# Kernel tuning notes

Hardware: AMD Instinct MI355X
Metric: run time of the kernel (lower is better)

Reference implementation:

```python
import jax, jax.numpy as jnp
import numpy as np

B, C, H, L, D = 128, 5, 50, 32, 300
VOCAB = 50000
KN = 20  # len(torch.arange(-0.9, 1.1, 0.1))
EPS = 1e-8


def setup_inputs() -> dict:
    key = jax.random.key(0)
    k1, k2, k3, k4 = jax.random.split(key, 4)
    return {
        "candidate_title": jax.random.randint(k1, (B, C, L), 0, VOCAB),
        "clicked_title": jax.random.randint(k2, (B, H, L), 0, VOCAB),
        "embedding": jax.random.normal(k3, (VOCAB, D), dtype=jnp.float32),
        "ltr_w": jax.random.normal(k4, (1, H * KN), dtype=jnp.float32) * 0.03,
        "ltr_b": jnp.zeros((1,), dtype=jnp.float32),
    }


def reference(candidate_title, clicked_title, embedding, ltr_w, ltr_b):
    mus = jnp.arange(KN, dtype=jnp.float32) * 0.1 - 0.9
    sigmas = jnp.concatenate([jnp.full((KN - 1,), 0.1, dtype=jnp.float32),
                              jnp.array([0.001], dtype=jnp.float32)])

    ce = embedding[candidate_title]            # [B,C,L,D]
    he = embedding[clicked_title]              # [B,H,L,D]
    # torch CosineSimilarity: dot / (clamp(||a||,eps)*clamp(||b||,eps))
    cn = ce / jnp.clip(jnp.linalg.norm(ce, axis=-1, keepdims=True), EPS)
    hn = he / jnp.clip(jnp.linalg.norm(he, axis=-1, keepdims=True), EPS)
    sim = jnp.einsum('bcid,bhjd->bchij', cn, hn)  # [B,C,H,L,L] fusion matrix

    # kernel pooling: sum over columns j per Gaussian kernel, then log-sum over rows i
    pooled = jnp.stack(
        [jnp.sum(jnp.exp(-(sim - mus[k]) ** 2 / (2.0 * sigmas[k] ** 2)), axis=-1)
         for k in range(KN)], axis=-1)          # [B,C,H,L,KN]
    pv = jnp.sum(jnp.log(jnp.clip(pooled, 1e-10)), axis=-2)  # [B,C,H,KN]
    pv = pv.reshape(B, C, H * KN)

    score = pv @ ltr_w.T + ltr_b               # [B,C,1]
    return jax.nn.log_softmax(score, axis=1)[..., 0]  # [B,C]
```

## Files before the change

kernel.cpp:

```cpp
#include <hip/hip_runtime.h>
#include <hip/hip_bf16.h>

#define VOCABN 50000
#define BN 128
#define CN 5
#define HN 50
#define LN 32
#define DN 300
#define DP 320
#define KNN 20

typedef __bf16    bf16x8 __attribute__((ext_vector_type(8)));
typedef float     f32x4  __attribute__((ext_vector_type(4)));
typedef float     f32x2  __attribute__((ext_vector_type(2)));
typedef ushort    u16x8  __attribute__((ext_vector_type(8)));

#if __has_builtin(__builtin_amdgcn_exp2f)
#define FEXP2 __builtin_amdgcn_exp2f
#else
#define FEXP2 exp2f
#endif
#if __has_builtin(__builtin_amdgcn_logf)
#define FLOG2 __builtin_amdgcn_logf
#else
#define FLOG2 log2f
#endif

#define LOG2E 1.4426950408889634f
#define LN2F  0.6931471805599453f

__global__ __launch_bounds__(256) void knorm_embed2(const float* __restrict__ emb,
                                                    ushort* __restrict__ tabo) {
    const int t    = threadIdx.x;
    const int lane = t & 63;
    const int w    = t >> 6;
    const int v    = blockIdx.x * 4 + w;
    const float* row = emb + (size_t)v * DN;
    const float4* r4 = (const float4*)row;

    float4 x = r4[lane];
    float ss = x.x * x.x + x.y * x.y + x.z * x.z + x.w * x.w;
    if (lane < 11) {
        float4 y = r4[64 + lane];
        ss += y.x * y.x + y.y * y.y + y.z * y.z + y.w * y.w;
    }
    #pragma unroll
    for (int off = 32; off; off >>= 1) ss += __shfl_xor(ss, off);
    const float scale = 1.0f / fmaxf(sqrtf(ss), 1e-8f);

    if (lane < 40) {
        u16x8 u;
        #pragma unroll
        for (int j = 0; j < 8; ++j) {
            int e = lane * 8 + j;
            float f = (e < DN) ? row[e] * scale : 0.f;
            __hip_bfloat16 h = __float2bfloat16(f);
            u[j] = *(ushort*)&h;
        }
        *(u16x8*)(tabo + (size_t)v * DP + lane * 8) = u;
    }
}

__device__ __forceinline__ int paddr(int row, int c) {
    return ((row >> 1) << 7) + ((((c + ((row & 1) << 2))) ^ ((row >> 1) & 7)) << 4);
}
__device__ __forceinline__ bf16x8 ldP(const ushort* buf, int row, int c) {
    return *(const bf16x8*)((const char*)buf + paddr(row, c));
}

__global__ __launch_bounds__(320, 4) void knrm_fused7(const int* __restrict__ cand,
                                                      const int* __restrict__ clik,
                                                      const ushort* __restrict__ tab,
                                                      const float* __restrict__ ltr_w,
                                                      float* __restrict__ score) {
    __shared__ __align__(16) ushort Abuf[2][80 * 64];
    __shared__ __align__(16) ushort Bbuf[2][32 * 64];
    __shared__ int tokA[160];
    __shared__ int tokB[64];

    const int t    = threadIdx.x;
    const int lane = t & 63;
    const int w    = t >> 6;
    const int bid  = (blockIdx.x & 7) * 400 + (blockIdx.x >> 3);
    const int b    = bid / 25;
    const int hg   = bid % 25;
    const int h0   = hg * 2;

    if (t < 160)      tokA[t] = cand[b * (CN * LN) + t];
    else if (t < 224) tokB[t - 160] = clik[b * (HN * LN) + h0 * LN + (t - 160)];
    __syncthreads();

    const int m15 = lane & 15;
    const int g4  = lane >> 4;

    const char* srcA[2]; int dstA[2];
    #pragma unroll
    for (int it = 0; it < 2; ++it) {
        int cid = it * 320 + t, ar = cid >> 2, c = cid & 3;
        srcA[it] = (const char*)tab + (size_t)tokA[ar] * (DP * 2) + c * 16;
        dstA[it] = paddr(ar, c);
    }
    const char* srcB; int dstB;
    {
        int tb = (t < 256) ? t : (t - 64);
        int ar = tb >> 2, c = tb & 3;
        srcB = (const char*)tab + (size_t)tokB[ar] * (DP * 2) + c * 16;
        dstB = paddr(ar, c);
    }

    f32x4 acc[2][4];
    #pragma unroll
    for (int at = 0; at < 2; ++at)
        #pragma unroll
        for (int jg = 0; jg < 4; ++jg)
            acc[at][jg] = (f32x4){0.f, 0.f, 0.f, 0.f};

    {
        int4 a0 = *(const int4*)(srcA[0]);
        int4 a1 = *(const int4*)(srcA[1]);
        int4 b0; if (t < 256) b0 = *(const int4*)(srcB);
        *(int4*)((char*)&Abuf[0][0] + dstA[0]) = a0;
        *(int4*)((char*)&Abuf[0][0] + dstA[1]) = a1;
        if (t < 256) *(int4*)((char*)&Bbuf[0][0] + dstB) = b0;
    }
    __syncthreads();

    #pragma unroll 2
    for (int ss = 0; ss < 10; ++ss) {
        const ushort* A = &Abuf[ss & 1][0];
        const ushort* B = &Bbuf[ss & 1][0];

        int4 a0, a1, b0;
        if (ss < 9) {
            const int so = (ss + 1) * 64;
            a0 = *(const int4*)(srcA[0] + so);
            a1 = *(const int4*)(srcA[1] + so);
            if (t < 256) b0 = *(const int4*)(srcB + so);
        }

        bf16x8 af0 = ldP(A, w * 32 + m15,      g4);
        bf16x8 af1 = ldP(A, w * 32 + 16 + m15, g4);
        #pragma unroll
        for (int jg = 0; jg < 4; ++jg) {
            bf16x8 bf = ldP(B, jg * 16 + m15, g4);
            acc[0][jg] = __builtin_amdgcn_mfma_f32_16x16x32_bf16(af0, bf, acc[0][jg], 0, 0, 0);
            acc[1][jg] = __builtin_amdgcn_mfma_f32_16x16x32_bf16(af1, bf, acc[1][jg], 0, 0, 0);
        }

        if (ss < 9) {
            char* An = (char*)&Abuf[(ss + 1) & 1][0];
            char* Bn = (char*)&Bbuf[(ss + 1) & 1][0];
            *(int4*)(An + dstA[0]) = a0;
            *(int4*)(An + dstA[1]) = a1;
            if (t < 256) *(int4*)(Bn + dstB) = b0;
            __syncthreads();
        }
    }

    const float C1   = 10.0f * LOG2E;
    const float C2   = -50.0f * LOG2E;
    const float AK19 = 849.3218002880191f;
    static const float CkT[10] = {
        1.0f, 0.6065306597126334f, 0.1353352832366127f, 0.011108996538242306f,
        3.3546262790251185e-4f, 3.7266531720786709e-6f, 1.5229979744712628e-8f,
        2.2897348456191135e-11f, 1.2664165549094176e-14f, 2.576757109154981e-18f };

    float* sb = (w < 4) ? ((float*)&Abuf[0][0] + w * (16 * 33))
                        : ((float*)&Bbuf[0][0]);
    const float* sp0 = sb + (lane >> 2) * 33 + (lane & 3) * 8;
    float res = 0.f;

    #pragma unroll
    for (int hl = 0; hl < 2; ++hl) {
        const float* wrow = ltr_w + (h0 + hl) * KNN;
        #pragma unroll
        for (int at = 0; at < 2; ++at) {
            #pragma unroll
            for (int r = 0; r < 4; ++r) {
                sb[(g4 * 4 + r) * 33 + m15]      = acc[at][hl * 2][r];
                sb[(g4 * 4 + r) * 33 + 16 + m15] = acc[at][hl * 2 + 1][r];
            }

            f32x2 Qp[9];
            #pragma unroll
            for (int j = 0; j < 9; ++j) Qp[j] = (f32x2){0.f, 0.f};
            float Q9 = 0.f, Q19 = 0.f;

            #pragma unroll
            for (int e = 0; e < 8; ++e) {
                float s  = sp0[e];
                float cs = C1 * s;
                float tt = FEXP2(cs);
                float uu = FEXP2(-cs);
                float e0 = FEXP2(C2 * (s * s));
                Q9 += e0;
                f32x2 tu = {tt, uu};
                f32x2 pm = {e0, e0};
                #pragma unroll
                for (int j = 0; j < 9; ++j) { pm *= tu; Qp[j] += pm; }
                float d = fmaf(s, AK19, -AK19);
                Q19 += FEXP2(-(d * d));
            }
            #pragma unroll
            for (int j = 0; j < 9; ++j) {
                Qp[j].x += __shfl_xor(Qp[j].x, 1); Qp[j].x += __shfl_xor(Qp[j].x, 2);
                Qp[j].y += __shfl_xor(Qp[j].y, 1); Qp[j].y += __shfl_xor(Qp[j].y, 2);
            }
            Q9  += __shfl_xor(Q9, 1);  Q9  += __shfl_xor(Q9, 2);
            Q19 += __shfl_xor(Q19, 1); Q19 += __shfl_xor(Q19, 2);

            float rs = wrow[9] * FLOG2(fmaxf(Q9, 1e-10f));
            #pragma unroll
            for (int j = 1; j <= 9; ++j) {
                rs += wrow[9 + j] * FLOG2(fmaxf(Qp[j - 1].x * CkT[j], 1e-10f));
                rs += wrow[9 - j] * FLOG2(fmaxf(Qp[j - 1].y * CkT[j], 1e-10f));
            }
            rs += wrow[19] * FLOG2(fmaxf(Q19, 1e-10f));
            res += rs;
        }
    }

    res *= 0.25f * LN2F;
    #pragma unroll
    for (int off = 32; off; off >>= 1) res += __shfl_xor(res, off);
    if (lane == 0) atomicAdd(&score[b * CN + w], res);
}

__global__ __launch_bounds__(128) void knrm_final(const float* __restrict__ score,
                                                  float* __restrict__ out) {
    int b = threadIdx.x;
    if (b < BN) {
        float s[CN];
        float m = -1e30f;
        #pragma unroll
        for (int c = 0; c < CN; ++c) { s[c] = score[b * CN + c]; m = fmaxf(m, s[c]); }
        float sum = 0.f;
        #pragma unroll
        for (int c = 0; c < CN; ++c) sum += FEXP2((s[c] - m) * LOG2E);
        float lse = m + FLOG2(sum) * LN2F;
        #pragma unroll
        for (int c = 0; c < CN; ++c) out[b * CN + c] = s[c] - lse;
    }
}

extern "C" void kernel_launch(void* const* d_in, const int* in_sizes, int n_in,
                              void* d_out, int out_size, void* d_ws, size_t ws_size,
                              hipStream_t stream) {
    const int*   cand  = (const int*)d_in[0];
    const int*   clik  = (const int*)d_in[1];
    const float* emb   = (const float*)d_in[2];
    const float* ltr_w = (const float*)d_in[3];
    float* out = (float*)d_out;

    const size_t TAB_B = (size_t)VOCABN * DP * 2;

    ushort* tab  = (ushort*)d_ws;
    float*  scre = (float*)((char*)d_ws + TAB_B);

    hipMemsetAsync(scre, 0, BN * CN * sizeof(float), stream);
    knorm_embed2<<<VOCABN / 4, 256, 0, stream>>>(emb, tab);
    knrm_fused7<<<BN * 25, 320, 0, stream>>>(cand, clik, tab, ltr_w, scre);
    knrm_final<<<1, 128, 0, stream>>>(scre, out);
}
```

Measured before the change: 129.6 us.

## Process one clicked title per block and split pooling rows across half-waves

Each block now handles a single clicked history title instead of two. That doubles the grid to BN*HN blocks, halves the B tile, per-thread accumulators and shared memory, and raises the launch-bounds occupancy hint from 4 to 6. The kernel-pooling epilogue is restructured so each of the 64 lanes reduces one full row over 16 columns with vectorized LDS reads, using one cross-half shuffle instead of 4-lane shuffle trees. In exchange, the candidate A tile is reloaded from global memory twice as often per clicked title, since the candidate tokens are re-gathered per block.

```diff
diff --git a/kernel.cpp b/kernel.cpp
--- a/kernel.cpp
+++ b/kernel.cpp
@@ -68,26 +68,28 @@
     return *(const bf16x8*)((const char*)buf + paddr(row, c));
 }
 
-__global__ __launch_bounds__(320, 4) void knrm_fused7(const int* __restrict__ cand,
+__global__ __launch_bounds__(320, 6) void knrm_fused8(const int* __restrict__ cand,
                                                       const int* __restrict__ clik,
                                                       const ushort* __restrict__ tab,
                                                       const float* __restrict__ ltr_w,
                                                       float* __restrict__ score) {
-    __shared__ __align__(16) ushort Abuf[2][80 * 64];
-    __shared__ __align__(16) ushort Bbuf[2][32 * 64];
-    __shared__ int tokA[160];
-    __shared__ int tokB[64];
+    __shared__ __align__(16) char smem[25344];
+    ushort* Abuf0 = (ushort*)smem;
+    ushort* Abuf1 = (ushort*)(smem + 10240);
+    ushort* Bbuf0 = (ushort*)(smem + 20480);
+    ushort* Bbuf1 = (ushort*)(smem + 22528);
+    int*    tokA  = (int*)(smem + 24576);
+    int*    tokB  = (int*)(smem + 25216);
 
     const int t    = threadIdx.x;
     const int lane = t & 63;
     const int w    = t >> 6;
-    const int bid  = (blockIdx.x & 7) * 400 + (blockIdx.x >> 3);
-    const int b    = bid / 25;
-    const int hg   = bid % 25;
-    const int h0   = hg * 2;
+    const int bid  = (blockIdx.x & 7) * 800 + (blockIdx.x >> 3);
+    const int b    = bid / HN;
+    const int h    = bid % HN;
 
     if (t < 160)      tokA[t] = cand[b * (CN * LN) + t];
-    else if (t < 224) tokB[t - 160] = clik[b * (HN * LN) + h0 * LN + (t - 160)];
+    else if (t < 192) tokB[t - 160] = clik[b * (HN * LN) + h * LN + (t - 160)];
     __syncthreads();
 
     const int m15 = lane & 15;
@@ -102,60 +104,61 @@
     }
     const char* srcB; int dstB;
     {
-        int tb = (t < 256) ? t : (t - 64);
+        int tb = t & 127;
         int ar = tb >> 2, c = tb & 3;
         srcB = (const char*)tab + (size_t)tokB[ar] * (DP * 2) + c * 16;
         dstB = paddr(ar, c);
     }
 
-    f32x4 acc[2][4];
+    f32x4 acc[2][2];
     #pragma unroll
     for (int at = 0; at < 2; ++at)
         #pragma unroll
-        for (int jg = 0; jg < 4; ++jg)
+        for (int jg = 0; jg < 2; ++jg)
             acc[at][jg] = (f32x4){0.f, 0.f, 0.f, 0.f};
 
     {
         int4 a0 = *(const int4*)(srcA[0]);
         int4 a1 = *(const int4*)(srcA[1]);
-        int4 b0; if (t < 256) b0 = *(const int4*)(srcB);
-        *(int4*)((char*)&Abuf[0][0] + dstA[0]) = a0;
-        *(int4*)((char*)&Abuf[0][0] + dstA[1]) = a1;
-        if (t < 256) *(int4*)((char*)&Bbuf[0][0] + dstB) = b0;
+        int4 b0; if (t < 128) b0 = *(const int4*)(srcB);
+        *(int4*)((char*)Abuf0 + dstA[0]) = a0;
+        *(int4*)((char*)Abuf0 + dstA[1]) = a1;
+        if (t < 128) *(int4*)((char*)Bbuf0 + dstB) = b0;
     }
     __syncthreads();
 
     #pragma unroll 2
     for (int ss = 0; ss < 10; ++ss) {
-        const ushort* A = &Abuf[ss & 1][0];
-        const ushort* B = &Bbuf[ss & 1][0];
+        const ushort* A = (ss & 1) ? Abuf1 : Abuf0;
+        const ushort* B = (ss & 1) ? Bbuf1 : Bbuf0;
 
         int4 a0, a1, b0;
         if (ss < 9) {
             const int so = (ss + 1) * 64;
             a0 = *(const int4*)(srcA[0] + so);
             a1 = *(const int4*)(srcA[1] + so);
-            if (t < 256) b0 = *(const int4*)(srcB + so);
+            if (t < 128) b0 = *(const int4*)(srcB + so);
         }
 
         bf16x8 af0 = ldP(A, w * 32 + m15,      g4);
         bf16x8 af1 = ldP(A, w * 32 + 16 + m15, g4);
-        #pragma unroll
-        for (int jg = 0; jg < 4; ++jg) {
-            bf16x8 bf = ldP(B, jg * 16 + m15, g4);
-            acc[0][jg] = __builtin_amdgcn_mfma_f32_16x16x32_bf16(af0, bf, acc[0][jg], 0, 0, 0);
-            acc[1][jg] = __builtin_amdgcn_mfma_f32_16x16x32_bf16(af1, bf, acc[1][jg], 0, 0, 0);
-        }
+        bf16x8 bf0 = ldP(B, m15,      g4);
+        bf16x8 bf1 = ldP(B, 16 + m15, g4);
+        acc[0][0] = __builtin_amdgcn_mfma_f32_16x16x32_bf16(af0, bf0, acc[0][0], 0, 0, 0);
+        acc[0][1] = __builtin_amdgcn_mfma_f32_16x16x32_bf16(af0, bf1, acc[0][1], 0, 0, 0);
+        acc[1][0] = __builtin_amdgcn_mfma_f32_16x16x32_bf16(af1, bf0, acc[1][0], 0, 0, 0);
+        acc[1][1] = __builtin_amdgcn_mfma_f32_16x16x32_bf16(af1, bf1, acc[1][1], 0, 0, 0);
 
         if (ss < 9) {
-            char* An = (char*)&Abuf[(ss + 1) & 1][0];
-            char* Bn = (char*)&Bbuf[(ss + 1) & 1][0];
+            char* An = (char*)((ss & 1) ? Abuf0 : Abuf1);
+            char* Bn = (char*)((ss & 1) ? Bbuf0 : Bbuf1);
             *(int4*)(An + dstA[0]) = a0;
             *(int4*)(An + dstA[1]) = a1;
-            if (t < 256) *(int4*)(Bn + dstB) = b0;
+            if (t < 128) *(int4*)(Bn + dstB) = b0;
             __syncthreads();
         }
     }
+    __syncthreads();
 
     const float C1   = 10.0f * LOG2E;
     const float C2   = -50.0f * LOG2E;
@@ -165,62 +168,64 @@
         3.3546262790251185e-4f, 3.7266531720786709e-6f, 1.5229979744712628e-8f,
         2.2897348456191135e-11f, 1.2664165549094176e-14f, 2.576757109154981e-18f };
 
-    float* sb = (w < 4) ? ((float*)&Abuf[0][0] + w * (16 * 33))
-                        : ((float*)&Bbuf[0][0]);
-    const float* sp0 = sb + (lane >> 2) * 33 + (lane & 3) * 8;
-    float res = 0.f;
-
-    #pragma unroll
-    for (int hl = 0; hl < 2; ++hl) {
-        const float* wrow = ltr_w + (h0 + hl) * KNN;
-        #pragma unroll
-        for (int at = 0; at < 2; ++at) {
+    float* sb = (float*)(smem + w * 4224);
+
+    #pragma unroll
+    for (int at = 0; at < 2; ++at)
+        #pragma unroll
+        for (int jgl = 0; jgl < 2; ++jgl)
             #pragma unroll
-            for (int r = 0; r < 4; ++r) {
-                sb[(g4 * 4 + r) * 33 + m15]      = acc[at][hl * 2][r];
-                sb[(g4 * 4 + r) * 33 + 16 + m15] = acc[at][hl * 2 + 1][r];
-            }
-
-            f32x2 Qp[9];
+            for (int r = 0; r < 4; ++r)
+                sb[(at * 16 + g4 * 4 + r) * 33 + jgl * 16 + m15] = acc[at][jgl][r];
+
+    const int hi = lane >> 5;
+    const float* sp = sb + (lane & 31) * 33 + hi * 16;
+
+    f32x2 Qp[9];
+    #pragma unroll
+    for (int j = 0; j < 9; ++j) Qp[j] = (f32x2){0.f, 0.f};
+    float Q9 = 0.f, Q19 = 0.f;
+
+    #pragma unroll
+    for (int ec = 0; ec < 4; ++ec) {
+        f32x4 v = *(const f32x4*)(sp + ec * 4);
+        #pragma unroll
+        for (int e = 0; e < 4; ++e) {
+            float s  = v[e];
+            float cs = C1 * s;
+            float tt = FEXP2(cs);
+            float uu = FEXP2(-cs);
+            float e0 = FEXP2(C2 * (s * s));
+            Q9 += e0;
+            f32x2 tu = {tt, uu};
+            f32x2 pm = {e0, e0};
             #pragma unroll
-            for (int j = 0; j < 9; ++j) Qp[j] = (f32x2){0.f, 0.f};
-            float Q9 = 0.f, Q19 = 0.f;
-
-            #pragma unroll
-            for (int e = 0; e < 8; ++e) {
-                float s  = sp0[e];
-                float cs = C1 * s;
-                float tt = FEXP2(cs);
-                float uu = FEXP2(-cs);
-                float e0 = FEXP2(C2 * (s * s));
-                Q9 += e0;
-                f32x2 tu = {tt, uu};
-                f32x2 pm = {e0, e0};
-                #pragma unroll
-                for (int j = 0; j < 9; ++j) { pm *= tu; Qp[j] += pm; }
-                float d = fmaf(s, AK19, -AK19);
-                Q19 += FEXP2(-(d * d));
-            }
-            #pragma unroll
-            for (int j = 0; j < 9; ++j) {
-                Qp[j].x += __shfl_xor(Qp[j].x, 1); Qp[j].x += __shfl_xor(Qp[j].x, 2);
-                Qp[j].y += __shfl_xor(Qp[j].y, 1); Qp[j].y += __shfl_xor(Qp[j].y, 2);
-            }
-            Q9  += __shfl_xor(Q9, 1);  Q9  += __shfl_xor(Q9, 2);
-            Q19 += __shfl_xor(Q19, 1); Q19 += __shfl_xor(Q19, 2);
-
-            float rs = wrow[9] * FLOG2(fmaxf(Q9, 1e-10f));
-            #pragma unroll
-            for (int j = 1; j <= 9; ++j) {
-                rs += wrow[9 + j] * FLOG2(fmaxf(Qp[j - 1].x * CkT[j], 1e-10f));
-                rs += wrow[9 - j] * FLOG2(fmaxf(Qp[j - 1].y * CkT[j], 1e-10f));
-            }
-            rs += wrow[19] * FLOG2(fmaxf(Q19, 1e-10f));
-            res += rs;
-        }
-    }
-
-    res *= 0.25f * LN2F;
+            for (int j = 0; j < 9; ++j) { pm *= tu; Qp[j] += pm; }
+            float d = fmaf(s, AK19, -AK19);
+            Q19 += FEXP2(-(d * d));
+        }
+    }
+
+    #pragma unroll
+    for (int j = 0; j < 9; ++j) {
+        Qp[j].x += __shfl_xor(Qp[j].x, 32);
+        Qp[j].y += __shfl_xor(Qp[j].y, 32);
+    }
+    Q9  += __shfl_xor(Q9, 32);
+    Q19 += __shfl_xor(Q19, 32);
+
+    const float* wrow = ltr_w + h * KNN;
+    float q0 = hi ? Q19 : Q9;
+    float w0 = wrow[hi ? 19 : 9];
+    float res = w0 * FLOG2(fmaxf(q0, 1e-10f));
+    #pragma unroll
+    for (int j = 1; j <= 9; ++j) {
+        float q  = hi ? Qp[j - 1].x : Qp[j - 1].y;
+        float wk = wrow[hi ? (9 + j) : (9 - j)];
+        res += wk * FLOG2(fmaxf(q * CkT[j], 1e-10f));
+    }
+
+    res *= LN2F;
     #pragma unroll
     for (int off = 32; off; off >>= 1) res += __shfl_xor(res, off);
     if (lane == 0) atomicAdd(&score[b * CN + w], res);
@@ -259,6 +264,6 @@
 
     hipMemsetAsync(scre, 0, BN * CN * sizeof(float), stream);
     knorm_embed2<<<VOCABN / 4, 256, 0, stream>>>(emb, tab);
-    knrm_fused7<<<BN * 25, 320, 0, stream>>>(cand, clik, tab, ltr_w, scre);
+    knrm_fused8<<<BN * HN, 320, 0, stream>>>(cand, clik, tab, ltr_w, scre);
     knrm_final<<<1, 128, 0, stream>>>(scre, out);
 }
```

New measurement: 131.5 us. About the same (+1.5%).
